# Kernel tuning notes

Measured on AMD Instinct MI355X. Metric: run time of the kernel, lower is better.

The kernel has to match this reference:

```python
import jax, jax.numpy as jnp
import numpy as np

EMBED_DIM = 1024
NUM_HEADS = 16
HEAD_DIM = EMBED_DIM // NUM_HEADS
ROPE_BASE = 10000.0


def setup_inputs() -> dict:
    key = jax.random.key(0)
    ks = jax.random.split(key, 9)
    B, S, E = 2, 2048, EMBED_DIM
    scale = 1.0 / np.sqrt(E)
    x = jax.random.normal(ks[0], (B, S, E), dtype=jnp.float32)
    Wq = jax.random.normal(ks[1], (E, E), dtype=jnp.float32) * scale
    bq = jnp.zeros((E,), dtype=jnp.float32)
    Wk = jax.random.normal(ks[2], (E, E), dtype=jnp.float32) * scale
    bk = jnp.zeros((E,), dtype=jnp.float32)
    Wv = jax.random.normal(ks[3], (E, E), dtype=jnp.float32) * scale
    bv = jnp.zeros((E,), dtype=jnp.float32)
    Wo = jax.random.normal(ks[4], (E, E), dtype=jnp.float32) * scale
    bo = jnp.zeros((E,), dtype=jnp.float32)
    return {"x": x, "Wq": Wq, "bq": bq, "Wk": Wk, "bk": bk,
            "Wv": Wv, "bv": bv, "Wo": Wo, "bo": bo}


def _rotary_emb(seq_len, dtype=jnp.float32):
    half = HEAD_DIM // 2
    inv_freq = 1.0 / (ROPE_BASE ** (jnp.arange(half, dtype=dtype) / half))
    pos = jnp.arange(seq_len, dtype=dtype)
    sinusoid = pos[:, None] * inv_freq[None, :]  # [S, half]
    sin = jnp.sin(sinusoid)
    cos = jnp.cos(sinusoid)
    # interleave-duplicate: (s0,s0,s1,s1,...) -> [S, HEAD_DIM]
    sin = jnp.stack((sin, sin), axis=-1).reshape(seq_len, HEAD_DIM)
    cos = jnp.stack((cos, cos), axis=-1).reshape(seq_len, HEAD_DIM)
    return sin, cos


def _rotate_half(x):
    x1 = x[..., ::2]
    x2 = x[..., 1::2]
    return jnp.stack((-x2, x1), axis=-1).reshape(x.shape)


def _apply_rope(x, sin, cos):
    # x: [B, H, S, D]; sin/cos: [S, D]
    return x * cos[None, None] + _rotate_half(x) * sin[None, None]


def reference(x, Wq, bq, Wk, bk, Wv, bv, Wo, bo):
    B, S, E = x.shape
    H, D = NUM_HEADS, HEAD_DIM

    def proj(W, b):
        t = x @ W.T + b  # [B, S, E]
        return t.reshape(B, S, H, D).transpose(0, 2, 1, 3)  # [B, H, S, D]

    q = proj(Wq, bq)
    k = proj(Wk, bk)
    v = proj(Wv, bv)

    sin, cos = _rotary_emb(S, x.dtype)
    q = _apply_rope(q, sin, cos)
    k = _apply_rope(k, sin, cos)

    scores = jnp.einsum("bhqd,bhkd->bhqk", q, k) / jnp.sqrt(jnp.asarray(D, x.dtype))
    causal = jnp.tril(jnp.ones((S, S), dtype=bool))  # keep lower triangle
    scores = jnp.where(causal[None, None], scores, -jnp.inf)
    weights = jax.nn.softmax(scores, axis=-1)
    out = jnp.einsum("bhqk,bhkd->bhqd", weights, v)
    out = out.transpose(0, 2, 1, 3).reshape(B, S, E)
    return out @ Wo.T + bo
```

## Files before the change

### kernel.cpp

```cpp
#include <hip/hip_runtime.h>
#include <hip/hip_bf16.h>
#include <cstdint>
#include <cstddef>

typedef __hip_bfloat16 bf16;
typedef __attribute__((ext_vector_type(8))) short bf16x8;
typedef __attribute__((ext_vector_type(4))) float f32x4;
typedef __attribute__((ext_vector_type(16))) float f32x16;

#define AS1C(p) ((const __attribute__((address_space(1))) void*)(p))
#define AS3(p)  ((__attribute__((address_space(3))) void*)(p))

constexpr int B_ = 2, S_ = 2048, E_ = 1024, H_ = 16, D_ = 64;
constexpr int M_ = B_ * S_;
constexpr float QSCALE_ = 0.125f * 1.44269504088896340736f;

__device__ __forceinline__ void gload_lds16(const bf16* g, bf16* l) {
  __builtin_amdgcn_global_load_lds(AS1C(g), AS3(l), 16, 0, 0);
}

__device__ __forceinline__ void cast4(const float* __restrict__ in, bf16* __restrict__ out, int i) {
  float4 v = reinterpret_cast<const float4*>(in)[i];
  union { bf16 b[4]; short4 s; } u;
  u.b[0] = __float2bfloat16(v.x);
  u.b[1] = __float2bfloat16(v.y);
  u.b[2] = __float2bfloat16(v.z);
  u.b[3] = __float2bfloat16(v.w);
  reinterpret_cast<short4*>(out)[i] = u.s;
}

__global__ void prep_kernel(const float* __restrict__ x,
                            const float* __restrict__ Wq, const float* __restrict__ Wk,
                            const float* __restrict__ Wv, const float* __restrict__ Wo,
                            const float* __restrict__ bq, const float* __restrict__ bk,
                            const float* __restrict__ bv,
                            bf16* __restrict__ xb, bf16* __restrict__ Wqkvb,
                            bf16* __restrict__ Wob, float* __restrict__ bqkv,
                            float* __restrict__ sintab, float* __restrict__ costab) {
  const int b = blockIdx.x, t = threadIdx.x;
  if (b < 4096) {
    cast4(x, xb, b * 256 + t);
  } else if (b < 5120) {
    cast4(Wo, Wob, (b - 4096) * 256 + t);
  } else if (b < 8192) {
    const int i = (b - 5120) * 256 + t;
    const int which = i >> 18;
    const int j = i & ((1 << 18) - 1);
    const float* src = which == 0 ? Wq : (which == 1 ? Wk : Wv);
    cast4(src, Wqkvb + (size_t)which * E_ * E_, j);
  } else if (b < 8448) {
    const int idx = (b - 8192) * 256 + t;
    const int s = idx >> 5, i = idx & 31;
    float inv = powf(10000.0f, -(float)i / 32.0f);
    float ang = (float)s * inv;
    sintab[idx] = sinf(ang);
    costab[idx] = cosf(ang);
  } else {
    for (int j = t; j < 768; j += 256) {
      const int which = j >> 8, jj = j & 255;
      const float* src = which == 0 ? bq : (which == 1 ? bk : bv);
      reinterpret_cast<float4*>(bqkv)[j] = reinterpret_cast<const float4*>(src)[jj];
    }
  }
}

__global__ __launch_bounds__(256)
void gemm_qkv(const bf16* __restrict__ A, const bf16* __restrict__ W,
              const float* __restrict__ bias,
              bf16* __restrict__ Qo, bf16* __restrict__ Ko, bf16* __restrict__ Vo,
              const float* __restrict__ sintab, const float* __restrict__ costab)
{
  constexpr int K = 1024, BK = 32;
  __shared__ __align__(16) bf16 smem[17408];
  const int tid = threadIdx.x;
  const int lane = tid & 63, wid = tid >> 6;
  const int g = lane >> 4, r16 = lane & 15;
  const int wr = wid >> 1, wc = wid & 1;
  const int swzr = (r16 >> 1) & 3;

  const int nwg = gridDim.x * gridDim.y;
  const int flat = blockIdx.y * gridDim.x + blockIdx.x;
  const int cpx = nwg >> 3;
  const int f2 = (flat & 7) * cpx + (flat >> 3);
  const int m0 = (f2 / gridDim.x) * 128, n0 = (f2 % gridDim.x) * 128;

  const f32x4 fz = {0.f, 0.f, 0.f, 0.f};
  f32x4 acc[4][4];
#pragma unroll
  for (int mi = 0; mi < 4; ++mi)
#pragma unroll
    for (int ni = 0; ni < 4; ++ni) acc[mi][ni] = fz;

  const bf16* Abase = A + (size_t)m0 * K;
  const bf16* Wbase = W + (size_t)n0 * K;
  const int c0 = tid, c1 = 256 + tid;
  const int r0c = c0 >> 2, cc0 = c0 & 3, sw0 = (r0c >> 1) & 3;
  const int r1c = c1 >> 2, cc1 = c1 & 3, sw1 = (r1c >> 1) & 3;

  auto stage = [&](int k0, int buf) {
    bf16* As = smem + buf * 4096;
    bf16* Bs = smem + 8192 + buf * 4096;
    gload_lds16(Abase + (size_t)r0c * K + k0 + ((cc0 ^ sw0) * 8), As + c0 * 8);
    gload_lds16(Abase + (size_t)r1c * K + k0 + ((cc1 ^ sw1) * 8), As + c1 * 8);
    gload_lds16(Wbase + (size_t)r0c * K + k0 + ((cc0 ^ sw0) * 8), Bs + c0 * 8);
    gload_lds16(Wbase + (size_t)r1c * K + k0 + ((cc1 ^ sw1) * 8), Bs + c1 * 8);
  };

  stage(0, 0);
  __syncthreads();
  int buf = 0;

  for (int k0 = 0; k0 < K; k0 += BK) {
    if (k0 + BK < K) stage(k0 + BK, buf ^ 1);

    const bf16* As = smem + buf * 4096;
    const bf16* Bs = smem + 8192 + buf * 4096;
    bf16x8 af[4], bfr[4];
#pragma unroll
    for (int mi = 0; mi < 4; ++mi)
      af[mi] = *reinterpret_cast<const bf16x8*>(
          As + (wr * 64 + mi * 16 + r16) * BK + 8 * (g ^ swzr));
#pragma unroll
    for (int ni = 0; ni < 4; ++ni)
      bfr[ni] = *reinterpret_cast<const bf16x8*>(
          Bs + (wc * 64 + ni * 16 + r16) * BK + 8 * (g ^ swzr));
    __builtin_amdgcn_s_setprio(1);
#pragma unroll
    for (int mi = 0; mi < 4; ++mi)
#pragma unroll
      for (int ni = 0; ni < 4; ++ni)
        acc[mi][ni] = __builtin_amdgcn_mfma_f32_16x16x32_bf16(af[mi], bfr[ni], acc[mi][ni], 0, 0, 0);
    __builtin_amdgcn_s_setprio(0);

    __syncthreads();
    buf ^= 1;
  }

  const int b = m0 >> 11;
  if (n0 >= 2048) {
#pragma unroll
    for (int mi = 0; mi < 4; ++mi) {
#pragma unroll
      for (int ni = 0; ni < 4; ++ni) {
        const int n_local = wc * 64 + ni * 16 + r16;
        const float bv = bias[n0 + n_local];
        const int m_base = wr * 64 + mi * 16 + g * 4;
        union { bf16 b4[4]; short4 s4; } u;
#pragma unroll
        for (int r = 0; r < 4; ++r) u.b4[r] = __float2bfloat16(acc[mi][ni][r] + bv);
        *reinterpret_cast<short4*>(&smem[n_local * 136 + m_base]) = u.s4;
      }
    }
    __syncthreads();
    const int srow0 = m0 & (S_ - 1);
#pragma unroll
    for (int i = 0; i < 8; ++i) {
      const int c = i * 256 + tid;
      const int row = c >> 4, cc = c & 15;
      const bf16x8 v = *reinterpret_cast<const bf16x8*>(&smem[row * 136 + cc * 8]);
      const int n = n0 + row;
      const int h = (n >> 6) & 15, d = n & 63;
      *reinterpret_cast<bf16x8*>(&Vo[((size_t)(b * H_ + h) * D_ + d) * S_ + srow0 + cc * 8]) = v;
    }
  } else {
#pragma unroll
    for (int mi = 0; mi < 4; ++mi) {
#pragma unroll
      for (int ni = 0; ni < 4; ++ni) {
        const int gn = n0 + wc * 64 + ni * 16 + r16;
        const float bv = bias[gn];
#pragma unroll
        for (int r = 0; r < 4; ++r) {
          const int gm = m0 + wr * 64 + mi * 16 + g * 4 + r;
          float val = acc[mi][ni][r] + bv;
          const int d = gn & 63;
          const int srow = gm & (S_ - 1);
          const float cs = costab[srow * 32 + (d >> 1)];
          const float sn = sintab[srow * 32 + (d >> 1)];
          const float pv = __shfl_xor(val, 1);
          val = (d & 1) ? (val * cs + pv * sn) : (val * cs - pv * sn);
          const int h = (gn >> 6) & 15;
          const size_t bh = (size_t)(b * H_ + h);
          if (gn < 1024) {
            Qo[(bh * S_ + srow) * D_ + d] = __float2bfloat16(val * QSCALE_);
          } else {
            Ko[(bh * S_ + srow) * D_ + d] = __float2bfloat16(val);
          }
        }
      }
    }
  }
}

__global__ __launch_bounds__(256)
void gemm_o(const bf16* __restrict__ A, const bf16* __restrict__ W,
            const float* __restrict__ bias, float* __restrict__ outF)
{
  constexpr int K = 1024, BK = 32;
  __shared__ __align__(16) bf16 As[2][64 * BK];
  __shared__ __align__(16) bf16 Bs[2][128 * BK];
  const int tid = threadIdx.x;
  const int lane = tid & 63;
  const int wc = tid >> 6;
  const int g = lane >> 4, r16 = lane & 15;
  const int swzr = (r16 >> 1) & 3;

  const int flat = blockIdx.x;
  const int f2 = (flat & 7) * 64 + (flat >> 3);
  const int m0 = (f2 >> 3) * 64, n0 = (f2 & 7) * 128;

  const f32x4 fz = {0.f, 0.f, 0.f, 0.f};
  f32x4 acc[4][2];
#pragma unroll
  for (int mi = 0; mi < 4; ++mi)
#pragma unroll
    for (int ni = 0; ni < 2; ++ni) acc[mi][ni] = fz;

  const bf16* Abase = A + (size_t)m0 * K;
  const bf16* Wbase = W + (size_t)n0 * K;
  const int c0 = tid, c1 = 256 + tid;
  const int r0c = c0 >> 2, cc0 = c0 & 3, sw0 = (r0c >> 1) & 3;
  const int r1c = c1 >> 2, cc1 = c1 & 3, sw1 = (r1c >> 1) & 3;

  auto stage = [&](int k0, int buf) {
    gload_lds16(Abase + (size_t)r0c * K + k0 + ((cc0 ^ sw0) * 8), As[buf] + c0 * 8);
    gload_lds16(Wbase + (size_t)r0c * K + k0 + ((cc0 ^ sw0) * 8), Bs[buf] + c0 * 8);
    gload_lds16(Wbase + (size_t)r1c * K + k0 + ((cc1 ^ sw1) * 8), Bs[buf] + c1 * 8);
  };

  stage(0, 0);
  __syncthreads();
  int buf = 0;

  for (int k0 = 0; k0 < K; k0 += BK) {
    if (k0 + BK < K) stage(k0 + BK, buf ^ 1);

    bf16x8 af[4], bfr[2];
#pragma unroll
    for (int mi = 0; mi < 4; ++mi)
      af[mi] = *reinterpret_cast<const bf16x8*>(
          As[buf] + (mi * 16 + r16) * BK + 8 * (g ^ swzr));
#pragma unroll
    for (int ni = 0; ni < 2; ++ni)
      bfr[ni] = *reinterpret_cast<const bf16x8*>(
          Bs[buf] + (wc * 32 + ni * 16 + r16) * BK + 8 * (g ^ swzr));
    __builtin_amdgcn_s_setprio(1);
#pragma unroll
    for (int mi = 0; mi < 4; ++mi)
#pragma unroll
      for (int ni = 0; ni < 2; ++ni)
        acc[mi][ni] = __builtin_amdgcn_mfma_f32_16x16x32_bf16(af[mi], bfr[ni], acc[mi][ni], 0, 0, 0);
    __builtin_amdgcn_s_setprio(0);

    __syncthreads();
    buf ^= 1;
  }

#pragma unroll
  for (int mi = 0; mi < 4; ++mi)
#pragma unroll
    for (int ni = 0; ni < 2; ++ni) {
      const int gn = n0 + wc * 32 + ni * 16 + r16;
      const float bv = bias[gn];
#pragma unroll
      for (int r = 0; r < 4; ++r) {
        const int gm = m0 + mi * 16 + g * 4 + r;
        outF[(size_t)gm * 1024 + gn] = acc[mi][ni][r] + bv;
      }
    }
}

__global__ __launch_bounds__(512)
void attn_kernel(const bf16* __restrict__ Q, const bf16* __restrict__ Kg,
                 const bf16* __restrict__ Vtg, bf16* __restrict__ Og)
{
  __shared__ __align__(16) bf16 Ks[2][2][64 * 64];
  __shared__ __align__(16) bf16 Vs[2][2][64 * 64];
  const int flat = blockIdx.x;
  const int bh = flat & 31;
  const int qblk = 15 - (flat >> 5);
  const int tid = threadIdx.x, lane = tid & 63, wid = tid >> 6;
  const int qg = wid & 3, ksl = wid >> 2;
  const int l31 = lane & 31, h = lane >> 5;
  const bf16* Qb = Q + (size_t)bh * S_ * D_;
  const bf16* Kb = Kg + (size_t)bh * S_ * D_;
  const bf16* Vb = Vtg + (size_t)bh * D_ * S_;
  const int b = bh >> 4, hd = bh & 15;
  bf16* Ob = Og + (size_t)b * S_ * E_ + hd * D_;

  const int q0 = qblk * 128;
  const int qw0 = q0 + qg * 32;
  const int nkt = 2 * qblk + 2;
  const int nsup = (nkt + 1) >> 1;

  bf16x8 qf[4];
#pragma unroll
  for (int i = 0; i < 4; ++i)
    qf[i] = *reinterpret_cast<const bf16x8*>(Qb + (size_t)(qw0 + l31) * 64 + 16 * i + 8 * h);

  f32x16 oacc0 = {};
  f32x16 oacc1 = {};
  float mrow = -__builtin_inff();
  float lrow = 0.f;

  auto stagepair = [&](int jp, int dbuf) {
    const int t0 = 2 * jp;
#pragma unroll
    for (int i = 0; i < 2; ++i) {
      const int kc = tid + 512 * i;
      const int tile = kc >> 9, c2 = kc & 511, r = c2 >> 3, cc = c2 & 7;
      gload_lds16(Kb + (size_t)((t0 + tile) * 64 + r) * 64 + ((cc ^ (r & 7)) * 8),
                  &Ks[dbuf][tile][c2 * 8]);
    }
#pragma unroll
    for (int i = 0; i < 2; ++i) {
      const int kc = tid + 512 * i;
      const int tile = kc >> 9, c2 = kc & 511, r = c2 >> 3, cc = c2 & 7;
      gload_lds16(Vb + (size_t)r * S_ + (t0 + tile) * 64 + ((cc ^ (r & 7)) * 8),
                  &Vs[dbuf][tile][c2 * 8]);
    }
  };

  stagepair(0, 0);
  __syncthreads();
  int cur = 0;

  for (int j = 0; j < nsup; ++j) {
    if (j + 1 < nsup) stagepair(j + 1, cur ^ 1);

    const int kt = 2 * j + ksl;
    if (kt < nkt) {
      const int k0 = kt * 64;
      if (k0 <= qw0 + 31) {
        const bf16* ksp = Ks[cur][ksl];
        const bf16* vsp = Vs[cur][ksl];
        f32x16 ps0 = {}, ps1 = {};
        __builtin_amdgcn_s_setprio(1);
#pragma unroll
        for (int i = 0; i < 4; ++i) {
          const bf16x8 ka0 = *reinterpret_cast<const bf16x8*>(
              &ksp[l31 * 64 + (((2 * i + h) ^ (l31 & 7)) * 8)]);
          ps0 = __builtin_amdgcn_mfma_f32_32x32x16_bf16(ka0, qf[i], ps0, 0, 0, 0);
        }
#pragma unroll
        for (int i = 0; i < 4; ++i) {
          const int row1 = 32 + l31;
          const bf16x8 ka1 = *reinterpret_cast<const bf16x8*>(
              &ksp[row1 * 64 + (((2 * i + h) ^ (row1 & 7)) * 8)]);
          ps1 = __builtin_amdgcn_mfma_f32_32x32x16_bf16(ka1, qf[i], ps1, 0, 0, 0);
        }
        __builtin_amdgcn_s_setprio(0);
        if (k0 + 63 > qw0) {
          const int qm = qw0 + l31 - k0;
#pragma unroll
          for (int r = 0; r < 16; ++r) {
            const int kl = (r & 3) + 8 * (r >> 2) + 4 * h;
            if (kl > qm) ps0[r] = -1e30f;
            if (32 + kl > qm) ps1[r] = -1e30f;
          }
        }
        float tm = ps0[0];
#pragma unroll
        for (int r = 1; r < 16; ++r) tm = fmaxf(tm, ps0[r]);
#pragma unroll
        for (int r = 0; r < 16; ++r) tm = fmaxf(tm, ps1[r]);
        tm = fmaxf(tm, __shfl_xor(tm, 32));
        if (__any((tm - mrow > 8.f) ? 1 : 0)) {
          const float mn = fmaxf(mrow, tm);
          const float scl = exp2f(mrow - mn);
          mrow = mn;
          lrow *= scl;
          float so[16];
#pragma unroll
          for (int r = 0; r < 16; ++r)
            so[r] = __shfl(scl, (r & 3) + 8 * (r >> 2) + 4 * h);
#pragma unroll
          for (int r = 0; r < 16; ++r) { oacc0[r] *= so[r]; oacc1[r] *= so[r]; }
        }
        float ssum = 0.f;
#pragma unroll
        for (int r = 0; r < 16; ++r) {
          const float p = exp2f(ps0[r] - mrow);
          ps0[r] = p; ssum += p;
        }
#pragma unroll
        for (int r = 0; r < 16; ++r) {
          const float p = exp2f(ps1[r] - mrow);
          ps1[r] = p; ssum += p;
        }
        lrow += ssum;
        unsigned int pk0[8], pk1[8];
#pragma unroll
        for (int i = 0; i < 8; ++i) {
          unsigned int r0, r1;
          asm("v_cvt_pk_bf16_f32 %0, %1, %2" : "=v"(r0) : "v"(ps0[2 * i]), "v"(ps0[2 * i + 1]));
          asm("v_cvt_pk_bf16_f32 %0, %1, %2" : "=v"(r1) : "v"(ps1[2 * i]), "v"(ps1[2 * i + 1]));
          pk0[i] = r0; pk1[i] = r1;
        }
#pragma unroll
        for (int ks = 0; ks < 4; ++ks) {
          const int ksq = ks & 1;
          unsigned int w0, w1, w2, w3;
          if (ks < 2) { w0 = pk0[4 * ksq]; w2 = pk0[4 * ksq + 2];
                        w1 = pk0[4 * ksq + 1]; w3 = pk0[4 * ksq + 3]; }
          else        { w0 = pk1[4 * ksq]; w2 = pk1[4 * ksq + 2];
                        w1 = pk1[4 * ksq + 1]; w3 = pk1[4 * ksq + 3]; }
          asm("v_permlane32_swap_b32 %0, %1" : "+v"(w0), "+v"(w2));
          asm("v_permlane32_swap_b32 %0, %1" : "+v"(w1), "+v"(w3));
          union { unsigned int w[4]; bf16x8 v; } Aw;
          Aw.w[0] = w0; Aw.w[1] = w1; Aw.w[2] = w2; Aw.w[3] = w3;
          const int sw = l31 & 7;
          const bf16x8 vf0 = *reinterpret_cast<const bf16x8*>(
              &vsp[l31 * 64 + (((2 * ks + h) ^ sw) * 8)]);
          const bf16x8 vf1 = *reinterpret_cast<const bf16x8*>(
              &vsp[(32 + l31) * 64 + (((2 * ks + h) ^ sw) * 8)]);
          __builtin_amdgcn_s_setprio(1);
          oacc0 = __builtin_amdgcn_mfma_f32_32x32x16_bf16(Aw.v, vf0, oacc0, 0, 0, 0);
          oacc1 = __builtin_amdgcn_mfma_f32_32x32x16_bf16(Aw.v, vf1, oacc1, 0, 0, 0);
          __builtin_amdgcn_s_setprio(0);
        }
      }
    }

    __syncthreads();
    cur ^= 1;
  }

  lrow += __shfl_xor(lrow, 32);

  float* Obuf = (float*)&Ks[0][0][0];
  float* mlb  = (float*)&Vs[0][0][0];
  if (ksl == 1) {
#pragma unroll
    for (int r = 0; r < 16; ++r) {
      const int crow = (r & 3) + 8 * (r >> 2) + 4 * h;
      Obuf[(qg * 32 + crow) * 64 + l31] = oacc0[r];
      Obuf[(qg * 32 + crow) * 64 + 32 + l31] = oacc1[r];
    }
    if (h == 0) {
      mlb[(qg * 32 + l31) * 2] = mrow;
      mlb[(qg * 32 + l31) * 2 + 1] = lrow;
    }
  }
  __syncthreads();
  if (ksl == 0) {
    const float pm = mlb[(qg * 32 + l31) * 2];
    const float pl = mlb[(qg * 32 + l31) * 2 + 1];
    const float mstar = fmaxf(mrow, pm);
    const float a = exp2f(mrow - mstar);
    const float bb = exp2f(pm - mstar);
    const float linv = 1.0f / (lrow * a + pl * bb);
    const float fa = a * linv, fb = bb * linv;
#pragma unroll
    for (int r = 0; r < 16; ++r) {
      const int crow = (r & 3) + 8 * (r >> 2) + 4 * h;
      const float far = __shfl(fa, crow);
      const float fbr = __shfl(fb, crow);
      const int qrow = qw0 + crow;
      const float o0 = oacc0[r] * far + Obuf[(qg * 32 + crow) * 64 + l31] * fbr;
      const float o1 = oacc1[r] * far + Obuf[(qg * 32 + crow) * 64 + 32 + l31] * fbr;
      Ob[(size_t)qrow * E_ + l31] = __float2bfloat16(o0);
      Ob[(size_t)qrow * E_ + 32 + l31] = __float2bfloat16(o1);
    }
  }
}

extern "C" void kernel_launch(void* const* d_in, const int* in_sizes, int n_in,
                              void* d_out, int out_size, void* d_ws, size_t ws_size,
                              hipStream_t stream) {
  const float* x  = (const float*)d_in[0];
  const float* Wq = (const float*)d_in[1];
  const float* bq = (const float*)d_in[2];
  const float* Wk = (const float*)d_in[3];
  const float* bk = (const float*)d_in[4];
  const float* Wv = (const float*)d_in[5];
  const float* bv = (const float*)d_in[6];
  const float* Wo = (const float*)d_in[7];
  const float* bo = (const float*)d_in[8];
  float* out = (float*)d_out;

  char* ws = (char*)d_ws;
  size_t off = 0;
  auto alloc = [&](size_t bytes) -> char* {
    char* p = ws + off; off += (bytes + 255) & ~(size_t)255; return p;
  };
  bf16* xb    = (bf16*)alloc((size_t)M_ * E_ * 2);
  bf16* Wqkvb = (bf16*)alloc((size_t)3 * E_ * E_ * 2);
  bf16* Wob   = (bf16*)alloc((size_t)E_ * E_ * 2);
  float* bqkv = (float*)alloc((size_t)3 * E_ * 4);
  bf16* Qb    = (bf16*)alloc((size_t)M_ * E_ * 2);
  bf16* Kb    = (bf16*)alloc((size_t)M_ * E_ * 2);
  bf16* Vtb   = (bf16*)alloc((size_t)M_ * E_ * 2);
  bf16* AOb   = (bf16*)alloc((size_t)M_ * E_ * 2);
  float* sintab = (float*)alloc((size_t)S_ * 32 * 4);
  float* costab = (float*)alloc((size_t)S_ * 32 * 4);

  prep_kernel<<<dim3(8449), 256, 0, stream>>>(x, Wq, Wk, Wv, Wo, bq, bk, bv,
                                              xb, Wqkvb, Wob, bqkv, sintab, costab);

  gemm_qkv<<<dim3(24, 32), 256, 0, stream>>>(xb, Wqkvb, bqkv, Qb, Kb, Vtb, sintab, costab);
  attn_kernel<<<dim3(512), 512, 0, stream>>>(Qb, Kb, Vtb, AOb);
  gemm_o<<<dim3(512), 256, 0, stream>>>(AOb, Wob, bo, out);
}
```

Before: 114.6 us.

## Triple-buffer GEMM LDS staging with partial vmcnt waits

Both projection GEMMs move from double to triple buffering of the LDS tiles, keeping two K-stages of global-to-LDS loads in flight. The full __syncthreads is replaced by an s_waitcnt vmcnt(N) that waits only for the oldest stage, followed by a raw barrier. This aims to hide global load latency behind the MFMA work. In exchange it uses more LDS, which may lower occupancy, and relies on hand-counted outstanding loads being correct.

```diff
diff --git a/kernel.cpp b/kernel.cpp
--- a/kernel.cpp
+++ b/kernel.cpp
@@ -70,8 +70,8 @@
               bf16* __restrict__ Qo, bf16* __restrict__ Ko, bf16* __restrict__ Vo,
               const float* __restrict__ sintab, const float* __restrict__ costab)
 {
-  constexpr int K = 1024, BK = 32;
-  __shared__ __align__(16) bf16 smem[17408];
+  constexpr int K = 1024, BK = 32, NS = 32;
+  __shared__ __align__(16) bf16 smem[24576];
   const int tid = threadIdx.x;
   const int lane = tid & 63, wid = tid >> 6;
   const int g = lane >> 4, r16 = lane & 15;
@@ -98,8 +98,8 @@
   const int r1c = c1 >> 2, cc1 = c1 & 3, sw1 = (r1c >> 1) & 3;
 
   auto stage = [&](int k0, int buf) {
-    bf16* As = smem + buf * 4096;
-    bf16* Bs = smem + 8192 + buf * 4096;
+    bf16* As = smem + buf * 8192;
+    bf16* Bs = As + 4096;
     gload_lds16(Abase + (size_t)r0c * K + k0 + ((cc0 ^ sw0) * 8), As + c0 * 8);
     gload_lds16(Abase + (size_t)r1c * K + k0 + ((cc1 ^ sw1) * 8), As + c1 * 8);
     gload_lds16(Wbase + (size_t)r0c * K + k0 + ((cc0 ^ sw0) * 8), Bs + c0 * 8);
@@ -107,14 +107,17 @@
   };
 
   stage(0, 0);
-  __syncthreads();
-  int buf = 0;
-
-  for (int k0 = 0; k0 < K; k0 += BK) {
-    if (k0 + BK < K) stage(k0 + BK, buf ^ 1);
-
-    const bf16* As = smem + buf * 4096;
-    const bf16* Bs = smem + 8192 + buf * 4096;
+  stage(BK, 1);
+  asm volatile("s_waitcnt vmcnt(4)" ::: "memory");
+  __builtin_amdgcn_s_barrier();
+  asm volatile("" ::: "memory");
+
+  for (int i = 0; i < NS; ++i) {
+    const bool more = (i + 2 < NS);
+    if (more) stage((i + 2) * BK, (i + 2) % 3);
+
+    const bf16* As = smem + (i % 3) * 8192;
+    const bf16* Bs = As + 4096;
     bf16x8 af[4], bfr[4];
 #pragma unroll
     for (int mi = 0; mi < 4; ++mi)
@@ -132,9 +135,14 @@
         acc[mi][ni] = __builtin_amdgcn_mfma_f32_16x16x32_bf16(af[mi], bfr[ni], acc[mi][ni], 0, 0, 0);
     __builtin_amdgcn_s_setprio(0);
 
-    __syncthreads();
-    buf ^= 1;
-  }
+    if (i + 1 < NS) {
+      if (more) asm volatile("s_waitcnt vmcnt(4)" ::: "memory");
+      else      asm volatile("s_waitcnt vmcnt(0)" ::: "memory");
+      __builtin_amdgcn_s_barrier();
+      asm volatile("" ::: "memory");
+    }
+  }
+  __syncthreads();
 
   const int b = m0 >> 11;
   if (n0 >= 2048) {
@@ -196,9 +204,8 @@
 void gemm_o(const bf16* __restrict__ A, const bf16* __restrict__ W,
             const float* __restrict__ bias, float* __restrict__ outF)
 {
-  constexpr int K = 1024, BK = 32;
-  __shared__ __align__(16) bf16 As[2][64 * BK];
-  __shared__ __align__(16) bf16 Bs[2][128 * BK];
+  constexpr int K = 1024, BK = 32, NS = 32;
+  __shared__ __align__(16) bf16 smem[18432];
   const int tid = threadIdx.x;
   const int lane = tid & 63;
   const int wc = tid >> 6;
@@ -223,27 +230,34 @@
   const int r1c = c1 >> 2, cc1 = c1 & 3, sw1 = (r1c >> 1) & 3;
 
   auto stage = [&](int k0, int buf) {
-    gload_lds16(Abase + (size_t)r0c * K + k0 + ((cc0 ^ sw0) * 8), As[buf] + c0 * 8);
-    gload_lds16(Wbase + (size_t)r0c * K + k0 + ((cc0 ^ sw0) * 8), Bs[buf] + c0 * 8);
-    gload_lds16(Wbase + (size_t)r1c * K + k0 + ((cc1 ^ sw1) * 8), Bs[buf] + c1 * 8);
+    bf16* As = smem + buf * 6144;
+    bf16* Bs = As + 2048;
+    gload_lds16(Abase + (size_t)r0c * K + k0 + ((cc0 ^ sw0) * 8), As + c0 * 8);
+    gload_lds16(Wbase + (size_t)r0c * K + k0 + ((cc0 ^ sw0) * 8), Bs + c0 * 8);
+    gload_lds16(Wbase + (size_t)r1c * K + k0 + ((cc1 ^ sw1) * 8), Bs + c1 * 8);
   };
 
   stage(0, 0);
-  __syncthreads();
-  int buf = 0;
-
-  for (int k0 = 0; k0 < K; k0 += BK) {
-    if (k0 + BK < K) stage(k0 + BK, buf ^ 1);
-
+  stage(BK, 1);
+  asm volatile("s_waitcnt vmcnt(3)" ::: "memory");
+  __builtin_amdgcn_s_barrier();
+  asm volatile("" ::: "memory");
+
+  for (int i = 0; i < NS; ++i) {
+    const bool more = (i + 2 < NS);
+    if (more) stage((i + 2) * BK, (i + 2) % 3);
+
+    const bf16* As = smem + (i % 3) * 6144;
+    const bf16* Bs = As + 2048;
     bf16x8 af[4], bfr[2];
 #pragma unroll
     for (int mi = 0; mi < 4; ++mi)
       af[mi] = *reinterpret_cast<const bf16x8*>(
-          As[buf] + (mi * 16 + r16) * BK + 8 * (g ^ swzr));
+          As + (mi * 16 + r16) * BK + 8 * (g ^ swzr));
 #pragma unroll
     for (int ni = 0; ni < 2; ++ni)
       bfr[ni] = *reinterpret_cast<const bf16x8*>(
-          Bs[buf] + (wc * 32 + ni * 16 + r16) * BK + 8 * (g ^ swzr));
+          Bs + (wc * 32 + ni * 16 + r16) * BK + 8 * (g ^ swzr));
     __builtin_amdgcn_s_setprio(1);
 #pragma unroll
     for (int mi = 0; mi < 4; ++mi)
@@ -252,8 +266,12 @@
         acc[mi][ni] = __builtin_amdgcn_mfma_f32_16x16x32_bf16(af[mi], bfr[ni], acc[mi][ni], 0, 0, 0);
     __builtin_amdgcn_s_setprio(0);
 
-    __syncthreads();
-    buf ^= 1;
+    if (i + 1 < NS) {
+      if (more) asm volatile("s_waitcnt vmcnt(3)" ::: "memory");
+      else      asm volatile("s_waitcnt vmcnt(0)" ::: "memory");
+      __builtin_amdgcn_s_barrier();
+      asm volatile("" ::: "memory");
+    }
   }
 
 #pragma unroll
```

Result: slower. 117.8 us (+2.8%).
